# Kernel optimization log

Measured on AMD Instinct MI355X. Metric: run time of the kernel, lower is better.

The kernel has to match this reference:

```python
import jax, jax.numpy as jnp
import numpy as np

B, F, H = 128, 12288, 2048   # batch, flattened-image dim (3x64x64), MLP hidden
TAU = 0.1                    # constraint(x) = relu(x@W1)@w2 - TAU  (so constraint(0) = -TAU < 0)
THRESHOLD = 1e-3
MAX_STEPS = 30


def setup_inputs() -> dict:
    key = jax.random.key(0)
    k1, k2, k3 = jax.random.split(key, 3)
    x0 = jnp.zeros((B, F), jnp.float32)                 # anchor point, constraint(x0) < 0 by construction
    x = jax.random.normal(k1, (B, F), jnp.float32)
    W1 = jax.random.normal(k2, (F, H), jnp.float32) / np.float32(np.sqrt(F))
    w2 = jax.random.normal(k3, (H,), jnp.float32) / np.float32(np.sqrt(H))
    return {"x0": x0, "x": x, "W1": W1, "w2": w2}


def reference(x0, x, W1, w2):
    def fvals(c):  # per-sample constraint value at interpolation coeff c: [B]
        xc = (1.0 - c)[:, None] * x0 + c[:, None] * x
        return jax.nn.relu(xc @ W1) @ w2 - TAU

    # f(0) = -TAU < 0 (asserted in original). Check f(1): samples already feasible skip search.
    f1 = fvals(jnp.ones((B,), jnp.float32))
    inside = f1 <= 0.0

    a = jnp.zeros((B,), jnp.float32)
    b = jnp.ones((B,), jnp.float32)
    c = jnp.ones((B,), jnp.float32)
    done = inside  # feasible samples keep c = 1 (projected == x)

    def step(carry, _):
        a, b, c, done = carry
        cm = (a + b) * 0.5
        v = fvals(cm)
        upd = ~done
        hit = upd & (v >= -THRESHOLD) & (v < 0.0)   # -threshold <= f(c) < 0 -> converged
        go_a = upd & (v < 0.0) & ~hit               # same sign as f(a): move a
        go_b = upd & (v >= 0.0)                     # opposite sign: move b
        a = jnp.where(go_a, cm, a)
        b = jnp.where(go_b, cm, b)
        c = jnp.where(upd, cm, c)                   # freeze c once done
        done = done | hit
        return (a, b, c, done), None

    (a, b, c, done), _ = jax.lax.scan(step, (a, b, c, done), None, length=MAX_STEPS)

    c = jnp.where(inside, 1.0, c)
    proj = (1.0 - c)[:, None] * x0 + c[:, None] * x
    # Original raises ConvergenceError -> NaN fill for non-converged samples.
    return jnp.where(done[:, None], proj, jnp.float32(jnp.nan))
```

## Files before the change

### kernel.cpp

```cpp
#include <hip/hip_runtime.h>
#include <hip/hip_bf16.h>

#define BB 128
#define FF 12288
#define HH 2048
#define TAU_F 0.1f
#define THR_F 1e-3f
#define NKG (FF / 8)
#define BH (BB * HH)
#define NFLAGS 192

typedef __attribute__((ext_vector_type(4))) float f32x4;
typedef __attribute__((ext_vector_type(8))) short s16x8;
typedef __attribute__((ext_vector_type(8))) unsigned short u16x8;

__device__ __forceinline__ void barrier_lds() {
    asm volatile("s_waitcnt lgkmcnt(0)\ns_barrier" ::: "memory");
}

__device__ __forceinline__ void bsplit(float v, unsigned short& h, unsigned short& l) {
    unsigned int u  = __float_as_uint(v);
    unsigned int rh = (u + 0x7fffu + ((u >> 16) & 1u)) >> 16;
    float hf = __uint_as_float(rh << 16);
    float lf = v - hf;
    unsigned int ul = __float_as_uint(lf);
    unsigned int rl = (ul + 0x7fffu + ((ul >> 16) & 1u)) >> 16;
    h = (unsigned short)rh;
    l = (unsigned short)rl;
}

__device__ __forceinline__ bool read_nz(const int* __restrict__ flags) {
    const int lane = threadIdx.x & 63;
    int v = 0;
    if (lane < NFLAGS / 4) {
        const int4 q = ((const int4*)flags)[lane];
        v = q.x | q.y | q.z | q.w;
    }
    return __any(v != 0);
}

__global__ __launch_bounds__(256) void presplit_kernel(
    const float* __restrict__ x, const float* __restrict__ x0,
    unsigned short* __restrict__ Ah, unsigned short* __restrict__ Al,
    int* __restrict__ flags) {
    const int z = blockIdx.y;
    const float* __restrict__ X = z ? x0 : x;
    unsigned short* AH = Ah + (size_t)z * NKG * BB * 8;
    unsigned short* AL = Al + (size_t)z * NKG * BB * 8;
    const int t = threadIdx.x;
    const int w = t >> 6, lane = t & 63;
    const int kg = blockIdx.x * 8 + (t & 7);
    __shared__ int snz[4];
    int tnz = 0;
#pragma unroll
    for (int r = 0; r < 4; ++r) {
        const int m = (t >> 3) + r * 32;
        const float* src = X + (size_t)m * FF + kg * 8;
        u16x8 hv, lv;
#pragma unroll
        for (int j = 0; j < 8; ++j) {
            const float v = src[j];
            tnz |= (v != 0.f);
            unsigned short h, lo;
            bsplit(v, h, lo);
            hv[j] = h; lv[j] = lo;
        }
        const size_t o = ((size_t)kg * BB + m) * 8;
        *(u16x8*)(AH + o) = hv;
        *(u16x8*)(AL + o) = lv;
    }
    if (z == 1) {
        const int wnz = __any(tnz != 0) ? 1 : 0;
        if (lane == 0) snz[w] = wnz;
        __syncthreads();
        if (t == 0) flags[blockIdx.x] = snz[0] | snz[1] | snz[2] | snz[3];
    }
}

__global__ __launch_bounds__(256, 4) void mfma_gemm_kernel(
    const unsigned short* __restrict__ Ah, const unsigned short* __restrict__ Al,
    const float* __restrict__ W1, float* __restrict__ P,
    const int* __restrict__ flags, int SK, int KC, int NIT) {
    const int z = blockIdx.y;
    if (z == 1 && !read_nz(flags)) return;

    const int nwg = gridDim.x;
    const int bx  = blockIdx.x;
    const int wg  = (bx & 7) * (nwg >> 3) + (bx >> 3);
    const int ct  = wg & 31;
    const int kc  = wg >> 5;

    const int t   = threadIdx.x;
    const int w   = t >> 6;
    const int l   = t & 63;
    const int kgl = l >> 4;
    const int li  = l & 15;

    __shared__ unsigned short lds[2][4096];

    const size_t zoffA = (size_t)z * NKG * BB * 8;
    const unsigned short* APH = Ah + zoffA;
    const unsigned short* APL = Al + zoffA;

    f32x4 acc[2][4];
#pragma unroll
    for (int mt = 0; mt < 2; ++mt)
#pragma unroll
        for (int nt = 0; nt < 4; ++nt) acc[mt][nt] = (f32x4)0.f;

    const int kbase = kc * KC;
    const int kg0   = kbase >> 3;
    const int bkg = t >> 6;
    const int bn  = t & 63;

    s16x8 ahE[2], alE[2], ahO[2], alO[2];
    auto loadA = [&](s16x8* ah, s16x8* al, int it) {
        const int kg = kg0 + it * 4 + kgl;
#pragma unroll
        for (int mt = 0; mt < 2; ++mt) {
            const size_t o = ((size_t)kg * BB + w * 32 + mt * 16 + li) * 8;
            ah[mt] = *(const s16x8*)(APH + o);
            al[mt] = *(const s16x8*)(APL + o);
        }
    };

    auto stageB_load = [&](int it, float* v) {
        const float* src = W1 + (size_t)(kbase + it * 32 + bkg * 8) * HH + ct * 64 + bn;
#pragma unroll
        for (int j = 0; j < 8; ++j) v[j] = src[(size_t)j * HH];
    };
    auto stageB_write = [&](int buf, const float* v) {
        u16x8 hv, lv;
#pragma unroll
        for (int j = 0; j < 8; ++j) {
            unsigned short h, lo;
            bsplit(v[j], h, lo);
            hv[j] = h; lv[j] = lo;
        }
        unsigned short* d = &lds[buf][(bkg * 64 + bn) * 8];
        *(u16x8*)(d)        = hv;
        *(u16x8*)(d + 2048) = lv;
    };
    auto computeR = [&](const s16x8* ah, const s16x8* al, int buf) {
        const unsigned short* L = lds[buf];
#pragma unroll
        for (int nt = 0; nt < 4; ++nt) {
            const int no = (kgl * 64 + nt * 16 + li) * 8;
            const s16x8 fbh = *(const s16x8*)&L[no];
            const s16x8 fbl = *(const s16x8*)&L[2048 + no];
#pragma unroll
            for (int mt = 0; mt < 2; ++mt) {
                acc[mt][nt] = __builtin_amdgcn_mfma_f32_16x16x32_bf16(ah[mt], fbh, acc[mt][nt], 0, 0, 0);
                acc[mt][nt] = __builtin_amdgcn_mfma_f32_16x16x32_bf16(ah[mt], fbl, acc[mt][nt], 0, 0, 0);
                acc[mt][nt] = __builtin_amdgcn_mfma_f32_16x16x32_bf16(al[mt], fbh, acc[mt][nt], 0, 0, 0);
            }
        }
    };

    float bv[8];
    loadA(ahE, alE, 0);
    stageB_load(0, bv);
    stageB_write(0, bv);
    barrier_lds();

    for (int it = 0; it < NIT; it += 2) {
        const bool m1 = (it + 1 < NIT);
        const bool m2 = (it + 2 < NIT);
        if (m1) { stageB_load(it + 1, bv); loadA(ahO, alO, it + 1); }
        computeR(ahE, alE, 0);
        if (m1) stageB_write(1, bv);
        barrier_lds();
        if (m1) {
            if (m2) { stageB_load(it + 2, bv); loadA(ahE, alE, it + 2); }
            computeR(ahO, alO, 1);
            if (m2) stageB_write(0, bv);
            barrier_lds();
        }
    }

    float* dst = P + (size_t)(z * SK + kc) * BH;
    const int r0 = w * 32 + (l >> 4) * 4;
    const int c0 = ct * 64 + li;
#pragma unroll
    for (int mt = 0; mt < 2; ++mt)
#pragma unroll
        for (int nt = 0; nt < 4; ++nt)
#pragma unroll
            for (int r = 0; r < 4; ++r)
                dst[(size_t)(r0 + mt * 16 + r) * HH + c0 + nt * 16] = acc[mt][nt][r];
}

__global__ __launch_bounds__(256) void zflags_kernel(
    const float4* __restrict__ x0, int* __restrict__ flags) {
    const int t = threadIdx.x;
    const int w = t >> 6, lane = t & 63;
    __shared__ int snz[4];
    int tnz = 0;
    const int base = blockIdx.x * 2048 + t;
#pragma unroll
    for (int j = 0; j < 8; ++j) {
        float4 v = x0[base + 256 * j];
        tnz |= (v.x != 0.f) | (v.y != 0.f) | (v.z != 0.f) | (v.w != 0.f);
    }
    const int wnz = __any(tnz != 0) ? 1 : 0;
    if (lane == 0) snz[w] = wnz;
    __syncthreads();
    if (t == 0) flags[blockIdx.x] = snz[0] | snz[1] | snz[2] | snz[3];
}

__global__ __launch_bounds__(256) void legacy_gemm_kernel(
    const float* __restrict__ x, const float* __restrict__ x0,
    const float* __restrict__ W1, float* __restrict__ P,
    const int* __restrict__ flags) {
    const int ct = blockIdx.x, z = blockIdx.z, t = threadIdx.x;
    if (z == 1 && !read_nz(flags)) return;
    const int cg = t & 7, rg = t >> 3;
    const int r0 = rg * 4, cc = ct * 64 + cg * 8;
    float acc[4][8];
#pragma unroll
    for (int i = 0; i < 4; ++i)
#pragma unroll
        for (int n = 0; n < 8; ++n) acc[i][n] = 0.f;
    const float* __restrict__ X = z ? x0 : x;
    for (int k = 0; k < FF; k += 4) {
        float xr[4][4];
#pragma unroll
        for (int i = 0; i < 4; ++i) {
            float4 v = *(const float4*)(X + (size_t)(r0 + i) * FF + k);
            xr[i][0] = v.x; xr[i][1] = v.y; xr[i][2] = v.z; xr[i][3] = v.w;
        }
        float wr[4][8];
#pragma unroll
        for (int j = 0; j < 4; ++j) {
            float4 a = *(const float4*)(W1 + (size_t)(k + j) * HH + cc);
            float4 b = *(const float4*)(W1 + (size_t)(k + j) * HH + cc + 4);
            wr[j][0] = a.x; wr[j][1] = a.y; wr[j][2] = a.z; wr[j][3] = a.w;
            wr[j][4] = b.x; wr[j][5] = b.y; wr[j][6] = b.z; wr[j][7] = b.w;
        }
#pragma unroll
        for (int j = 0; j < 4; ++j)
#pragma unroll
            for (int i = 0; i < 4; ++i)
#pragma unroll
                for (int n = 0; n < 8; ++n)
                    acc[i][n] = fmaf(xr[i][j], wr[j][n], acc[i][n]);
    }
    float* Pp = P + (size_t)z * BH;
#pragma unroll
    for (int i = 0; i < 4; ++i) {
        float4 o0, o1;
        o0.x = acc[i][0]; o0.y = acc[i][1]; o0.z = acc[i][2]; o0.w = acc[i][3];
        o1.x = acc[i][4]; o1.y = acc[i][5]; o1.z = acc[i][6]; o1.w = acc[i][7];
        *(float4*)(Pp + (size_t)(r0 + i) * HH + cc) = o0;
        *(float4*)(Pp + (size_t)(r0 + i) * HH + cc + 4) = o1;
    }
}

__global__ __launch_bounds__(1024) void bisect_write_kernel(
    const float* __restrict__ P, const float* __restrict__ w2,
    const float* __restrict__ x, const float* __restrict__ x0,
    const int* __restrict__ flags, float* __restrict__ out, int SK) {
    const int b = blockIdx.x;
    const int t = threadIdx.x;
    const int w = t >> 6;
    const int lane = t & 63;
    __shared__ float red[16];
    const bool nz = read_nz(flags);

    const float2* P1 = (const float2*)(P + (size_t)b * HH) + t;
    float2 u1 = {0.f, 0.f};
    for (int kc = 0; kc < SK; ++kc) {
        const float2 v = P1[(size_t)kc * (BH / 2)];
        u1.x += v.x; u1.y += v.y;
    }
    const float2 wv = ((const float2*)w2)[t];

    auto blockReduce = [&](float v) -> float {
#pragma unroll
        for (int off = 32; off > 0; off >>= 1) v += __shfl_xor(v, off);
        if (lane == 0) red[w] = v;
        __syncthreads();
        float s = 0.f;
#pragma unroll
        for (int i = 0; i < 16; ++i) s += red[i];
        __syncthreads();
        return s;
    };

    float c = 1.f;
    bool done = false;
    if (!nz) {
        float p = fmaf(fmaxf(u1.x, 0.f), wv.x, fmaxf(u1.y, 0.f) * wv.y);
        const float S = blockReduce(p);
        const float f1 = S - TAU_F;
        const bool inside = (f1 <= 0.f);
        float a = 0.f, bh = 1.f;
        done = inside;
        for (int it = 0; it < 30; ++it) {
            const float cm = 0.5f * (a + bh);
            const float v = cm * S - TAU_F;
            const bool upd  = !done;
            const bool hit  = upd && (v >= -THR_F) && (v < 0.f);
            const bool go_a = upd && (v < 0.f) && !hit;
            const bool go_b = upd && (v >= 0.f);
            a  = go_a ? cm : a;
            bh = go_b ? cm : bh;
            c  = upd  ? cm : c;
            done = done || hit;
        }
        c = inside ? 1.f : c;
    } else {
        const float2* P0 = (const float2*)(P + (size_t)(SK * BH) + (size_t)b * HH) + t;
        float2 u0 = {0.f, 0.f};
        for (int kc = 0; kc < SK; ++kc) {
            const float2 v = P0[(size_t)kc * (BH / 2)];
            u0.x += v.x; u0.y += v.y;
        }
        const float2 dd = {u1.x - u0.x, u1.y - u0.y};
        auto feval = [&](float cc) -> float {
            float p = fmaf(fmaxf(fmaf(cc, dd.x, u0.x), 0.f), wv.x,
                           fmaxf(fmaf(cc, dd.y, u0.y), 0.f) * wv.y);
            return blockReduce(p) - TAU_F;
        };
        const float f1 = feval(1.f);
        const bool inside = (f1 <= 0.f);
        float a = 0.f, bh = 1.f;
        done = inside;
        for (int it = 0; it < 30; ++it) {
            const float cm = 0.5f * (a + bh);
            const float v = feval(cm);
            const bool upd  = !done;
            const bool hit  = upd && (v >= -THR_F) && (v < 0.f);
            const bool go_a = upd && (v < 0.f) && !hit;
            const bool go_b = upd && (v >= 0.f);
            a  = go_a ? cm : a;
            bh = go_b ? cm : bh;
            c  = upd  ? cm : c;
            done = done || hit;
        }
        c = inside ? 1.f : c;
    }

    const float nanv = __int_as_float(0x7fc00000);
    const float4* xr  = (const float4*)(x  + (size_t)b * FF);
    const float4* x0r = (const float4*)(x0 + (size_t)b * FF);
    float4* orow = (float4*)(out + (size_t)b * FF);
    if (!done) {
        float4 o; o.x = o.y = o.z = o.w = nanv;
#pragma unroll
        for (int k2 = 0; k2 < 3; ++k2) orow[t + 1024 * k2] = o;
    } else if (!nz) {
#pragma unroll
        for (int k2 = 0; k2 < 3; ++k2) {
            const int i = t + 1024 * k2;
            float4 xv = xr[i], o;
            o.x = c * xv.x; o.y = c * xv.y; o.z = c * xv.z; o.w = c * xv.w;
            orow[i] = o;
        }
    } else {
#pragma unroll
        for (int k2 = 0; k2 < 3; ++k2) {
            const int i = t + 1024 * k2;
            float4 xv = xr[i], zv = x0r[i], o;
            o.x = fmaf(c, xv.x - zv.x, zv.x);
            o.y = fmaf(c, xv.y - zv.y, zv.y);
            o.z = fmaf(c, xv.z - zv.z, zv.z);
            o.w = fmaf(c, xv.w - zv.w, zv.w);
            orow[i] = o;
        }
    }
}

extern "C" void kernel_launch(void* const* d_in, const int* in_sizes, int n_in,
                              void* d_out, int out_size, void* d_ws, size_t ws_size,
                              hipStream_t stream) {
    const float* x0 = (const float*)d_in[0];
    const float* x  = (const float*)d_in[1];
    const float* W1 = (const float*)d_in[2];
    const float* w2 = (const float*)d_in[3];
    float* out = (float*)d_out;
    char* ws = (char*)d_ws;

    const size_t szA   = (size_t)2 * NKG * BB * 8 * sizeof(unsigned short);
    const size_t offAl = szA;
    const size_t offFl = 2 * szA;
    const size_t offP  = offFl + 1024;

    int SK = 0;
    const int cand[5] = {24, 12, 6, 3, 1};
    for (int i = 0; i < 5; ++i) {
        const size_t need = offP + (size_t)2 * cand[i] * BH * sizeof(float);
        if (ws_size >= need) { SK = cand[i]; break; }
    }

    if (SK > 0) {
        unsigned short* Ah = (unsigned short*)ws;
        unsigned short* Al = (unsigned short*)(ws + offAl);
        int*   flags = (int*)(ws + offFl);
        float* P     = (float*)(ws + offP);
        const int KC = FF / SK, NIT = KC / 32;

        presplit_kernel<<<dim3(NKG / 8, 2), 256, 0, stream>>>(x, x0, Ah, Al, flags);
        mfma_gemm_kernel<<<dim3(32 * SK, 2), 256, 0, stream>>>(Ah, Al, W1, P, flags, SK, KC, NIT);
        bisect_write_kernel<<<BB, 1024, 0, stream>>>(P, w2, x, x0, flags, out, SK);
    } else {
        float* P     = (float*)ws;
        int*   flags = (int*)(ws + (size_t)2 * BH * sizeof(float));
        zflags_kernel<<<NFLAGS, 256, 0, stream>>>((const float4*)x0, flags);
        legacy_gemm_kernel<<<dim3(32, 1, 2), 256, 0, stream>>>(x, x0, W1, P, flags);
        bisect_write_kernel<<<BB, 1024, 0, stream>>>(P, w2, x, x0, flags, out, 1);
    }
}
```

Before: 50.53 us.

## Skip zero x0 blocks in presplit and GEMM, deepen W1 prefetch, retune split-K

The presplit kernel now checks each x0 block for nonzero values before splitting it. The GEMM zero-fills A fragments for blocks flagged as zero instead of loading them. W1 staging is double-buffered in registers so loads run two iterations ahead, and launch bounds move to two waves per SIMD. Split-K candidates change from 24/12/6/3 to 16/8/4/2. Together these aim to cut memory traffic for the all-zero anchor and hide W1 load latency, at the cost of more registers and one fewer split-K level of parallelism.

```diff
diff --git a/kernel.cpp b/kernel.cpp
--- a/kernel.cpp
+++ b/kernel.cpp
@@ -9,6 +9,7 @@
 #define NKG (FF / 8)
 #define BH (BB * HH)
 #define NFLAGS 192
+#define SKD 16
 
 typedef __attribute__((ext_vector_type(4))) float f32x4;
 typedef __attribute__((ext_vector_type(8))) short s16x8;
@@ -39,45 +40,62 @@
     return __any(v != 0);
 }
 
+__device__ __forceinline__ void presplit_blk(
+    const float* __restrict__ X, unsigned short* __restrict__ AH,
+    unsigned short* __restrict__ AL, int i, int t) {
+    const int kg = i * 8 + (t & 7);
+#pragma unroll
+    for (int r = 0; r < 4; ++r) {
+        const int m = (t >> 3) + r * 32;
+        const float* src = X + (size_t)m * FF + kg * 8;
+        u16x8 hv, lv;
+#pragma unroll
+        for (int j = 0; j < 8; ++j) {
+            unsigned short h, lo;
+            bsplit(src[j], h, lo);
+            hv[j] = h; lv[j] = lo;
+        }
+        const size_t o = ((size_t)kg * BB + m) * 8;
+        *(u16x8*)(AH + o) = hv;
+        *(u16x8*)(AL + o) = lv;
+    }
+}
+
 __global__ __launch_bounds__(256) void presplit_kernel(
     const float* __restrict__ x, const float* __restrict__ x0,
     unsigned short* __restrict__ Ah, unsigned short* __restrict__ Al,
     int* __restrict__ flags) {
     const int z = blockIdx.y;
-    const float* __restrict__ X = z ? x0 : x;
-    unsigned short* AH = Ah + (size_t)z * NKG * BB * 8;
-    unsigned short* AL = Al + (size_t)z * NKG * BB * 8;
+    const int i = blockIdx.x;
     const int t = threadIdx.x;
+    if (z == 0) {
+        presplit_blk(x, Ah, Al, i, t);
+        return;
+    }
+    __shared__ int snz[4];
     const int w = t >> 6, lane = t & 63;
-    const int kg = blockIdx.x * 8 + (t & 7);
-    __shared__ int snz[4];
+    const int kg = i * 8 + (t & 7);
     int tnz = 0;
 #pragma unroll
     for (int r = 0; r < 4; ++r) {
         const int m = (t >> 3) + r * 32;
-        const float* src = X + (size_t)m * FF + kg * 8;
-        u16x8 hv, lv;
-#pragma unroll
-        for (int j = 0; j < 8; ++j) {
-            const float v = src[j];
-            tnz |= (v != 0.f);
-            unsigned short h, lo;
-            bsplit(v, h, lo);
-            hv[j] = h; lv[j] = lo;
-        }
-        const size_t o = ((size_t)kg * BB + m) * 8;
-        *(u16x8*)(AH + o) = hv;
-        *(u16x8*)(AL + o) = lv;
-    }
-    if (z == 1) {
-        const int wnz = __any(tnz != 0) ? 1 : 0;
-        if (lane == 0) snz[w] = wnz;
-        __syncthreads();
-        if (t == 0) flags[blockIdx.x] = snz[0] | snz[1] | snz[2] | snz[3];
-    }
-}
-
-__global__ __launch_bounds__(256, 4) void mfma_gemm_kernel(
+        const float4* src = (const float4*)(x0 + (size_t)m * FF + kg * 8);
+        const float4 a = src[0], b = src[1];
+        tnz |= (a.x != 0.f) | (a.y != 0.f) | (a.z != 0.f) | (a.w != 0.f)
+             | (b.x != 0.f) | (b.y != 0.f) | (b.z != 0.f) | (b.w != 0.f);
+    }
+    const int wnz = __any(tnz != 0) ? 1 : 0;
+    if (lane == 0) snz[w] = wnz;
+    __syncthreads();
+    const int bnz = snz[0] | snz[1] | snz[2] | snz[3];
+    if (t == 0) flags[i] = bnz;
+    if (bnz) {
+        const size_t zoff = (size_t)NKG * BB * 8;
+        presplit_blk(x0, Ah + zoff, Al + zoff, i, t);
+    }
+}
+
+__global__ __launch_bounds__(256, 2) void mfma_gemm_kernel(
     const unsigned short* __restrict__ Ah, const unsigned short* __restrict__ Al,
     const float* __restrict__ W1, float* __restrict__ P,
     const int* __restrict__ flags, int SK, int KC, int NIT) {
@@ -101,6 +119,7 @@
     const size_t zoffA = (size_t)z * NKG * BB * 8;
     const unsigned short* APH = Ah + zoffA;
     const unsigned short* APL = Al + zoffA;
+    const bool zchk = (z == 1);
 
     f32x4 acc[2][4];
 #pragma unroll
@@ -116,6 +135,11 @@
     s16x8 ahE[2], alE[2], ahO[2], alO[2];
     auto loadA = [&](s16x8* ah, s16x8* al, int it) {
         const int kg = kg0 + it * 4 + kgl;
+        if (zchk && flags[kg >> 3] == 0) {
+#pragma unroll
+            for (int mt = 0; mt < 2; ++mt) { ah[mt] = (s16x8)0; al[mt] = (s16x8)0; }
+            return;
+        }
 #pragma unroll
         for (int mt = 0; mt < 2; ++mt) {
             const size_t o = ((size_t)kg * BB + w * 32 + mt * 16 + li) * 8;
@@ -157,23 +181,27 @@
         }
     };
 
-    float bv[8];
+    float bvE[8], bvO[8];
     loadA(ahE, alE, 0);
-    stageB_load(0, bv);
-    stageB_write(0, bv);
+    stageB_load(0, bvE);
+    stageB_write(0, bvE);
+    if (NIT > 1) stageB_load(1, bvO);
     barrier_lds();
 
     for (int it = 0; it < NIT; it += 2) {
         const bool m1 = (it + 1 < NIT);
         const bool m2 = (it + 2 < NIT);
-        if (m1) { stageB_load(it + 1, bv); loadA(ahO, alO, it + 1); }
+        const bool m3 = (it + 3 < NIT);
+        if (m2) stageB_load(it + 2, bvE);
+        if (m1) loadA(ahO, alO, it + 1);
         computeR(ahE, alE, 0);
-        if (m1) stageB_write(1, bv);
+        if (m1) stageB_write(1, bvO);
         barrier_lds();
         if (m1) {
-            if (m2) { stageB_load(it + 2, bv); loadA(ahE, alE, it + 2); }
+            if (m3) stageB_load(it + 3, bvO);
+            if (m2) loadA(ahE, alE, it + 2);
             computeR(ahO, alO, 1);
-            if (m2) stageB_write(0, bv);
+            if (m2) stageB_write(0, bvE);
             barrier_lds();
         }
     }
@@ -190,70 +218,23 @@
                 dst[(size_t)(r0 + mt * 16 + r) * HH + c0 + nt * 16] = acc[mt][nt][r];
 }
 
-__global__ __launch_bounds__(256) void zflags_kernel(
-    const float4* __restrict__ x0, int* __restrict__ flags) {
-    const int t = threadIdx.x;
-    const int w = t >> 6, lane = t & 63;
-    __shared__ int snz[4];
-    int tnz = 0;
-    const int base = blockIdx.x * 2048 + t;
-#pragma unroll
-    for (int j = 0; j < 8; ++j) {
-        float4 v = x0[base + 256 * j];
-        tnz |= (v.x != 0.f) | (v.y != 0.f) | (v.z != 0.f) | (v.w != 0.f);
-    }
-    const int wnz = __any(tnz != 0) ? 1 : 0;
-    if (lane == 0) snz[w] = wnz;
-    __syncthreads();
-    if (t == 0) flags[blockIdx.x] = snz[0] | snz[1] | snz[2] | snz[3];
-}
-
-__global__ __launch_bounds__(256) void legacy_gemm_kernel(
-    const float* __restrict__ x, const float* __restrict__ x0,
-    const float* __restrict__ W1, float* __restrict__ P,
-    const int* __restrict__ flags) {
-    const int ct = blockIdx.x, z = blockIdx.z, t = threadIdx.x;
-    if (z == 1 && !read_nz(flags)) return;
-    const int cg = t & 7, rg = t >> 3;
-    const int r0 = rg * 4, cc = ct * 64 + cg * 8;
-    float acc[4][8];
-#pragma unroll
-    for (int i = 0; i < 4; ++i)
-#pragma unroll
-        for (int n = 0; n < 8; ++n) acc[i][n] = 0.f;
-    const float* __restrict__ X = z ? x0 : x;
-    for (int k = 0; k < FF; k += 4) {
-        float xr[4][4];
-#pragma unroll
-        for (int i = 0; i < 4; ++i) {
-            float4 v = *(const float4*)(X + (size_t)(r0 + i) * FF + k);
-            xr[i][0] = v.x; xr[i][1] = v.y; xr[i][2] = v.z; xr[i][3] = v.w;
-        }
-        float wr[4][8];
-#pragma unroll
-        for (int j = 0; j < 4; ++j) {
-            float4 a = *(const float4*)(W1 + (size_t)(k + j) * HH + cc);
-            float4 b = *(const float4*)(W1 + (size_t)(k + j) * HH + cc + 4);
-            wr[j][0] = a.x; wr[j][1] = a.y; wr[j][2] = a.z; wr[j][3] = a.w;
-            wr[j][4] = b.x; wr[j][5] = b.y; wr[j][6] = b.z; wr[j][7] = b.w;
-        }
-#pragma unroll
-        for (int j = 0; j < 4; ++j)
-#pragma unroll
-            for (int i = 0; i < 4; ++i)
-#pragma unroll
-                for (int n = 0; n < 8; ++n)
-                    acc[i][n] = fmaf(xr[i][j], wr[j][n], acc[i][n]);
-    }
-    float* Pp = P + (size_t)z * BH;
-#pragma unroll
-    for (int i = 0; i < 4; ++i) {
-        float4 o0, o1;
-        o0.x = acc[i][0]; o0.y = acc[i][1]; o0.z = acc[i][2]; o0.w = acc[i][3];
-        o1.x = acc[i][4]; o1.y = acc[i][5]; o1.z = acc[i][6]; o1.w = acc[i][7];
-        *(float4*)(Pp + (size_t)(r0 + i) * HH + cc) = o0;
-        *(float4*)(Pp + (size_t)(r0 + i) * HH + cc + 4) = o1;
-    }
+__device__ __forceinline__ void solve_linear(float S, float& c, bool& done) {
+    const bool inside = (S - TAU_F <= 0.f);
+    float a = 0.f, bh = 1.f;
+    c = 1.f; done = inside;
+    for (int it = 0; it < 30; ++it) {
+        const float cm = 0.5f * (a + bh);
+        const float v = cm * S - TAU_F;
+        const bool upd  = !done;
+        const bool hit  = upd && (v >= -THR_F) && (v < 0.f);
+        const bool go_a = upd && (v < 0.f) && !hit;
+        const bool go_b = upd && (v >= 0.f);
+        a  = go_a ? cm : a;
+        bh = go_b ? cm : bh;
+        c  = upd  ? cm : c;
+        done = done || hit;
+    }
+    c = inside ? 1.f : c;
 }
 
 __global__ __launch_bounds__(1024) void bisect_write_kernel(
@@ -292,23 +273,7 @@
     if (!nz) {
         float p = fmaf(fmaxf(u1.x, 0.f), wv.x, fmaxf(u1.y, 0.f) * wv.y);
         const float S = blockReduce(p);
-        const float f1 = S - TAU_F;
-        const bool inside = (f1 <= 0.f);
-        float a = 0.f, bh = 1.f;
-        done = inside;
-        for (int it = 0; it < 30; ++it) {
-            const float cm = 0.5f * (a + bh);
-            const float v = cm * S - TAU_F;
-            const bool upd  = !done;
-            const bool hit  = upd && (v >= -THR_F) && (v < 0.f);
-            const bool go_a = upd && (v < 0.f) && !hit;
-            const bool go_b = upd && (v >= 0.f);
-            a  = go_a ? cm : a;
-            bh = go_b ? cm : bh;
-            c  = upd  ? cm : c;
-            done = done || hit;
-        }
-        c = inside ? 1.f : c;
+        solve_linear(S, c, done);
     } else {
         const float2* P0 = (const float2*)(P + (size_t)(SK * BH) + (size_t)b * HH) + t;
         float2 u0 = {0.f, 0.f};
@@ -371,6 +336,72 @@
     }
 }
 
+__global__ __launch_bounds__(256) void zflags_kernel(
+    const float4* __restrict__ x0, int* __restrict__ flags) {
+    const int t = threadIdx.x;
+    const int w = t >> 6, lane = t & 63;
+    __shared__ int snz[4];
+    int tnz = 0;
+    const int base = blockIdx.x * 2048 + t;
+#pragma unroll
+    for (int j = 0; j < 8; ++j) {
+        float4 v = x0[base + 256 * j];
+        tnz |= (v.x != 0.f) | (v.y != 0.f) | (v.z != 0.f) | (v.w != 0.f);
+    }
+    const int wnz = __any(tnz != 0) ? 1 : 0;
+    if (lane == 0) snz[w] = wnz;
+    __syncthreads();
+    if (t == 0) flags[blockIdx.x] = snz[0] | snz[1] | snz[2] | snz[3];
+}
+
+__global__ __launch_bounds__(256) void legacy_gemm_kernel(
+    const float* __restrict__ x, const float* __restrict__ x0,
+    const float* __restrict__ W1, float* __restrict__ P,
+    const int* __restrict__ flags) {
+    const int ct = blockIdx.x, z = blockIdx.z, t = threadIdx.x;
+    if (z == 1 && !read_nz(flags)) return;
+    const int cg = t & 7, rg = t >> 3;
+    const int r0 = rg * 4, cc = ct * 64 + cg * 8;
+    float acc[4][8];
+#pragma unroll
+    for (int i = 0; i < 4; ++i)
+#pragma unroll
+        for (int n = 0; n < 8; ++n) acc[i][n] = 0.f;
+    const float* __restrict__ X = z ? x0 : x;
+    for (int k = 0; k < FF; k += 4) {
+        float xr[4][4];
+#pragma unroll
+        for (int i = 0; i < 4; ++i) {
+            float4 v = *(const float4*)(X + (size_t)(r0 + i) * FF + k);
+            xr[i][0] = v.x; xr[i][1] = v.y; xr[i][2] = v.z; xr[i][3] = v.w;
+        }
+        float wr[4][8];
+#pragma unroll
+        for (int j = 0; j < 4; ++j) {
+            float4 a = *(const float4*)(W1 + (size_t)(k + j) * HH + cc);
+            float4 b = *(const float4*)(W1 + (size_t)(k + j) * HH + cc + 4);
+            wr[j][0] = a.x; wr[j][1] = a.y; wr[j][2] = a.z; wr[j][3] = a.w;
+            wr[j][4] = b.x; wr[j][5] = b.y; wr[j][6] = b.z; wr[j][7] = b.w;
+        }
+#pragma unroll
+        for (int j = 0; j < 4; ++j)
+#pragma unroll
+            for (int i = 0; i < 4; ++i)
+#pragma unroll
+                for (int n = 0; n < 8; ++n)
+                    acc[i][n] = fmaf(xr[i][j], wr[j][n], acc[i][n]);
+    }
+    float* Pp = P + (size_t)z * BH;
+#pragma unroll
+    for (int i = 0; i < 4; ++i) {
+        float4 o0, o1;
+        o0.x = acc[i][0]; o0.y = acc[i][1]; o0.z = acc[i][2]; o0.w = acc[i][3];
+        o1.x = acc[i][4]; o1.y = acc[i][5]; o1.z = acc[i][6]; o1.w = acc[i][7];
+        *(float4*)(Pp + (size_t)(r0 + i) * HH + cc) = o0;
+        *(float4*)(Pp + (size_t)(r0 + i) * HH + cc + 4) = o1;
+    }
+}
+
 extern "C" void kernel_launch(void* const* d_in, const int* in_sizes, int n_in,
                               void* d_out, int out_size, void* d_ws, size_t ws_size,
                               hipStream_t stream) {
@@ -387,7 +418,7 @@
     const size_t offP  = offFl + 1024;
 
     int SK = 0;
-    const int cand[5] = {24, 12, 6, 3, 1};
+    const int cand[5] = {SKD, 8, 4, 2, 1};
     for (int i = 0; i < 5; ++i) {
         const size_t need = offP + (size_t)2 * cand[i] * BH * sizeof(float);
         if (ws_size >= need) { SK = cand[i]; break; }
@@ -400,7 +431,7 @@
         float* P     = (float*)(ws + offP);
         const int KC = FF / SK, NIT = KC / 32;
 
-        presplit_kernel<<<dim3(NKG / 8, 2), 256, 0, stream>>>(x, x0, Ah, Al, flags);
+        presplit_kernel<<<dim3(NFLAGS, 2), 256, 0, stream>>>(x, x0, Ah, Al, flags);
         mfma_gemm_kernel<<<dim3(32 * SK, 2), 256, 0, stream>>>(Ah, Al, W1, P, flags, SK, KC, NIT);
         bisect_write_kernel<<<BB, 1024, 0, stream>>>(P, w2, x, x0, flags, out, SK);
     } else {
```

Result: no change. 49.69 us (-1.7%).
